# Kernel tuning notes

Measured on AMD Instinct MI355X. Metric: run time of the kernel, lower is better.

## Reference

```python
import jax, jax.numpy as jnp
import numpy as np

N = 100000       # nodes
E = 1600000      # edges
F_IN = 128       # input features
HID = 64         # hidden dim
CLS = 16         # classes


def setup_inputs() -> dict:
    key = jax.random.key(0)
    k = jax.random.split(key, 6)
    x = jax.random.normal(k[0], (N, F_IN), dtype=jnp.float32)
    src = jax.random.randint(k[1], (E,), 0, N, dtype=jnp.int32)
    dst = jax.random.randint(k[2], (E,), 0, N, dtype=jnp.int32)
    edge_index = jnp.stack([src, dst], axis=0)
    W1 = jax.random.normal(k[3], (F_IN, HID), dtype=jnp.float32) * (1.0 / np.sqrt(F_IN))
    b1 = jnp.zeros((HID,), dtype=jnp.float32)
    W2 = jax.random.normal(k[4], (HID, CLS), dtype=jnp.float32) * (1.0 / np.sqrt(HID))
    b2 = jnp.zeros((CLS,), dtype=jnp.float32)
    return {"x": x, "edge_index": edge_index, "W1": W1, "b1": b1, "W2": W2, "b2": b2}


def gcn_conv(x, W, b, src, dst, n_nodes):
    # GCNConv(normalize=True): h = W x; out_i = sum_{j->i} h_j / sqrt(d_i d_j) + h_i / d_i + b
    # (self-loops added with weight 1; deg includes the self-loop)
    h = x @ W                                             # [N, out]
    ones = jnp.ones(src.shape[0], dtype=x.dtype)
    deg = jax.ops.segment_sum(ones, dst, num_segments=n_nodes) + 1.0   # [N]
    dinv = deg ** -0.5
    norm = dinv[src] * dinv[dst]                          # [E]
    msg = h[src] * norm[:, None]                          # [E, out] gather
    out = jax.ops.segment_sum(msg, dst, num_segments=n_nodes)          # scatter-add
    out = out + h * (1.0 / deg)[:, None] + b              # self-loop term + bias
    return out


def reference(x, edge_index, W1, b1, W2, b2):
    src, dst = edge_index[0], edge_index[1]
    n = x.shape[0]
    h = jax.nn.relu(gcn_conv(x, W1, b1, src, dst, n))
    # dropout(p=0.5) is identity in eval mode
    h = jax.nn.relu(gcn_conv(h, W2, b2, src, dst, n))
    return jax.nn.log_softmax(h, axis=-1)
```

## Files before the change

kernel.cpp:

```cpp
#include <hip/hip_runtime.h>
#include <hip/hip_bf16.h>


typedef unsigned short u16;
typedef __attribute__((ext_vector_type(8))) short short8;
typedef __attribute__((ext_vector_type(4))) float f32x4;

#define CAP 4096

__device__ __forceinline__ float bf2f(u16 u) {
  return __uint_as_float(((unsigned int)u) << 16);
}
__device__ __forceinline__ u16 f2bf(float f) {
  unsigned int u = __float_as_uint(f);
  u += 0x7fffu + ((u >> 16) & 1u);
  return (u16)(u >> 16);
}

__global__ __launch_bounds__(256) void kconvw(const void* __restrict__ W1r,
                                              const void* __restrict__ b1r,
                                              const void* __restrict__ W2r,
                                              const void* __restrict__ b2r,
                                              u16* __restrict__ W1b,
                                              float* __restrict__ b1f,
                                              u16* __restrict__ W2b,
                                              float* __restrict__ b2f,
                                              int* __restrict__ mode) {
  __shared__ float red[4];
  __shared__ int smode;
  const u16* w = (const u16*)W1r;
  float mx = 0.f;
  for (int i = threadIdx.x; i < 8192; i += 256) {
    float av = fabsf(bf2f(w[i]));
    if (!(av <= 1e6f)) av = 3e38f;
    mx = fmaxf(mx, av);
  }
  #pragma unroll
  for (int off = 32; off >= 1; off >>= 1) mx = fmaxf(mx, __shfl_xor(mx, off, 64));
  if ((threadIdx.x & 63) == 0) red[threadIdx.x >> 6] = mx;
  __syncthreads();
  if (threadIdx.x == 0) {
    float m2 = fmaxf(fmaxf(red[0], red[1]), fmaxf(red[2], red[3]));
    smode = (m2 > 1e6f) ? 1 : 0;
    if (blockIdx.x == 0) mode[0] = smode;
  }
  __syncthreads();
  int m = smode;
  int gid = blockIdx.x * 256 + threadIdx.x, stride = gridDim.x * 256;
  for (int i = gid; i < 8192; i += stride)
    W1b[i] = m ? f2bf(((const float*)W1r)[i]) : ((const u16*)W1r)[i];
  for (int i = gid; i < 1024; i += stride)
    W2b[i] = m ? f2bf(((const float*)W2r)[i]) : ((const u16*)W2r)[i];
  for (int i = gid; i < 64; i += stride)
    b1f[i] = m ? ((const float*)b1r)[i] : bf2f(((const u16*)b1r)[i]);
  for (int i = gid; i < 16; i += stride)
    b2f[i] = m ? ((const float*)b2r)[i] : bf2f(((const u16*)b2r)[i]);
}

__global__ __launch_bounds__(512) void kpart(const int* __restrict__ src,
                                             const int* __restrict__ dst,
                                             int* __restrict__ cursor,
                                             int* __restrict__ etmp,
                                             int E, int NB) {
  __shared__ int hist[1024], basep[1024];
  int tid = threadIdx.x;
  for (int i = tid; i < 1024; i += 512) hist[i] = 0;
  __syncthreads();
  int e0 = blockIdx.x * 8192 + tid * 16;
  int pk[16], off[16], cb[16];
  if (e0 + 15 < E) {
    int4 s4[4], d4[4];
    #pragma unroll
    for (int u = 0; u < 4; ++u) {
      s4[u] = ((const int4*)(src + e0))[u];
      d4[u] = ((const int4*)(dst + e0))[u];
    }
    const int* sp = (const int*)s4;
    const int* dp = (const int*)d4;
    #pragma unroll
    for (int k = 0; k < 16; ++k) {
      int s = sp[k], d = dp[k];
      cb[k] = d >> 7;
      pk[k] = (s << 7) | (d & 127);
      off[k] = atomicAdd(&hist[cb[k]], 1);
    }
  } else {
    #pragma unroll
    for (int k = 0; k < 16; ++k) {
      int e = e0 + k;
      cb[k] = -1;
      if (e < E) {
        int s = src[e], d = dst[e];
        cb[k] = d >> 7;
        pk[k] = (s << 7) | (d & 127);
        off[k] = atomicAdd(&hist[cb[k]], 1);
      }
    }
  }
  __syncthreads();
  for (int i = tid; i < NB; i += 512)
    if (hist[i]) basep[i] = atomicAdd(&cursor[i], hist[i]);
  __syncthreads();
  if (e0 + 15 < E) {
    #pragma unroll
    for (int k = 0; k < 16; ++k)
      etmp[cb[k] * CAP + basep[cb[k]] + off[k]] = pk[k];
  } else {
    #pragma unroll
    for (int k = 0; k < 16; ++k)
      if (cb[k] >= 0) etmp[cb[k] * CAP + basep[cb[k]] + off[k]] = pk[k];
  }
}

__global__ __launch_bounds__(512) void kfine(const int* __restrict__ etmp,
                                             const int* __restrict__ cursor,
                                             float* __restrict__ dinv, int N) {
  __shared__ int hist[128];
  int bk = blockIdx.x, tid = threadIdx.x;
  int cnt = cursor[bk], base = bk * CAP;
  if (tid < 128) hist[tid] = 0;
  __syncthreads();
  for (int i = tid; i < cnt; i += 512)
    atomicAdd(&hist[etmp[base + i] & 127], 1);
  __syncthreads();
  int node = (bk << 7) + tid;
  if (tid < 128 && node < N)
    dinv[node] = rsqrtf((float)(hist[tid] + 1));
}

__global__ __launch_bounds__(256) void kgemm1(const void* __restrict__ xraw,
                                              const u16* __restrict__ W1b,
                                              const int* __restrict__ mode,
                                              const float* __restrict__ dinv,
                                              u16* __restrict__ h1s, int n) {
  int mflag = mode[0];
  int wid = blockIdx.x * 4 + (threadIdx.x >> 6);
  int row0 = wid * 16;
  if (row0 >= n) return;
  int lane = threadIdx.x & 63;
  int m = lane & 15, q = lane >> 4;

  short8 bfrag[4][4];
  for (int jb = 0; jb < 4; ++jb)
    for (int kb = 0; kb < 4; ++kb) {
      short8 f;
      #pragma unroll
      for (int j = 0; j < 8; ++j)
        f[j] = (short)W1b[(kb * 32 + q * 8 + j) * 64 + jb * 16 + m];
      bfrag[jb][kb] = f;
    }

  f32x4 acc[4];
  #pragma unroll
  for (int jb = 0; jb < 4; ++jb) acc[jb] = (f32x4){0.f, 0.f, 0.f, 0.f};

  #pragma unroll
  for (int kb = 0; kb < 4; ++kb) {
    short8 a;
    if (mflag) {
      const float* xf = (const float*)xraw + (size_t)(row0 + m) * 128 + kb * 32 + q * 8;
      float4 u0 = ((const float4*)xf)[0];
      float4 u1 = ((const float4*)xf)[1];
      __hip_bfloat162 p0 = __float22bfloat162_rn(make_float2(u0.x, u0.y));
      __hip_bfloat162 p1 = __float22bfloat162_rn(make_float2(u0.z, u0.w));
      __hip_bfloat162 p2 = __float22bfloat162_rn(make_float2(u1.x, u1.y));
      __hip_bfloat162 p3 = __float22bfloat162_rn(make_float2(u1.z, u1.w));
      unsigned int w0 = *(const unsigned int*)&p0;
      unsigned int w1 = *(const unsigned int*)&p1;
      unsigned int w2 = *(const unsigned int*)&p2;
      unsigned int w3 = *(const unsigned int*)&p3;
      a[0] = (short)(w0 & 0xffff); a[1] = (short)(w0 >> 16);
      a[2] = (short)(w1 & 0xffff); a[3] = (short)(w1 >> 16);
      a[4] = (short)(w2 & 0xffff); a[5] = (short)(w2 >> 16);
      a[6] = (short)(w3 & 0xffff); a[7] = (short)(w3 >> 16);
    } else {
      a = *(const short8*)((const u16*)xraw + (size_t)(row0 + m) * 128 + kb * 32 + q * 8);
    }
    #pragma unroll
    for (int jb = 0; jb < 4; ++jb)
      acc[jb] = __builtin_amdgcn_mfma_f32_16x16x32_bf16(a, bfrag[jb][kb], acc[jb], 0, 0, 0);
  }

  #pragma unroll
  for (int r = 0; r < 4; ++r) {
    float dv = dinv[row0 + q * 4 + r];
    #pragma unroll
    for (int jb = 0; jb < 4; ++jb)
      h1s[(row0 + q * 4 + r) * 64 + jb * 16 + m] = f2bf(acc[jb][r] * dv);
  }
}

__global__ __launch_bounds__(512) void kagg1f(
    const u16* __restrict__ h1s, const int* __restrict__ etmp,
    const int* __restrict__ cursor, const float* __restrict__ dinv,
    const float* __restrict__ b1f, const u16* __restrict__ W2b,
    int* __restrict__ esort, int2* __restrict__ rowse,
    u16* __restrict__ h2sb, int N) {
  __shared__ int eL[CAP];
  __shared__ int eS[CAP];
  __shared__ int hist[128], starts[128], curs[128];
  __shared__ float sdinv[128];

  int tid = threadIdx.x;
  int bk = blockIdx.x;
  int base = bk * CAP;
  int cnt = cursor[bk];
  int node0 = bk << 7;

  if (tid < 128) {
    hist[tid] = 0;
    int nd = node0 + tid;
    sdinv[tid] = (nd < N) ? dinv[nd] : 0.f;
  }
  __syncthreads();
  for (int i = tid; i < cnt; i += 512) {
    int pk = etmp[base + i];
    eL[i] = pk;
    atomicAdd(&hist[pk & 127], 1);
  }
  __syncthreads();
  if (tid < 64) {
    int v0 = hist[tid], v1 = hist[tid + 64];
    int s0 = v0;
    #pragma unroll
    for (int off = 1; off < 64; off <<= 1) {
      int t = __shfl_up(s0, off, 64);
      if (tid >= off) s0 += t;
    }
    int tot0 = __shfl(s0, 63, 64);
    int s1 = v1;
    #pragma unroll
    for (int off = 1; off < 64; off <<= 1) {
      int t = __shfl_up(s1, off, 64);
      if (tid >= off) s1 += t;
    }
    s1 += tot0;
    int e0x = s0 - v0, e1x = s1 - v1;
    starts[tid] = e0x;  curs[tid] = e0x;
    starts[tid + 64] = e1x;  curs[tid + 64] = e1x;
    int n0 = node0 + tid, n1 = n0 + 64;
    if (n0 < N) rowse[n0] = make_int2(base + e0x, base + e0x + v0);
    if (n1 < N) rowse[n1] = make_int2(base + e1x, base + e1x + v1);
  }
  __syncthreads();
  for (int i = tid; i < cnt; i += 512) {
    int pk = eL[i];
    int pos = atomicAdd(&curs[pk & 127], 1);
    int sidx = pk >> 7;
    eS[pos] = sidx;
    esort[base + pos] = sidx;
  }

  int lane = tid & 63, wv = tid >> 6;
  int m16 = lane & 15, q = lane >> 4;
  short8 bw0, bw1;
  #pragma unroll
  for (int j = 0; j < 8; ++j) {
    bw0[j] = (short)W2b[(q * 8 + j) * 16 + m16];
    bw1[j] = (short)W2b[(32 + q * 8 + j) * 16 + m16];
  }
  __syncthreads();

  float* rowsL = (float*)eL;
  const uint2* h1v = (const uint2*)h1s;
  int ql = m16;

  for (int pass = 0; pass < 4; ++pass) {
    int nl = pass * 32 + wv * 4 + q;
    int nd = node0 + nl;
    int cn = (nd < N) ? nd : node0;
    int rs = starts[nl], deg = hist[nl];
    float a0 = 0.f, a1 = 0.f, a2 = 0.f, a3 = 0.f;
    int k = rs, ke = rs + deg;
    for (; k + 8 <= ke; k += 8) {
      int sI[8];
      uint2 g[8];
      #pragma unroll
      for (int p = 0; p < 8; ++p) sI[p] = eS[k + p];
      #pragma unroll
      for (int p = 0; p < 8; ++p) g[p] = h1v[sI[p] * 16 + ql];
      #pragma unroll
      for (int p = 0; p < 8; ++p) {
        a0 += bf2f((u16)(g[p].x & 0xffff));
        a1 += bf2f((u16)(g[p].x >> 16));
        a2 += bf2f((u16)(g[p].y & 0xffff));
        a3 += bf2f((u16)(g[p].y >> 16));
      }
    }
    for (; k < ke; ++k) {
      int s = eS[k];
      uint2 g = h1v[s * 16 + ql];
      a0 += bf2f((u16)(g.x & 0xffff));
      a1 += bf2f((u16)(g.x >> 16));
      a2 += bf2f((u16)(g.y & 0xffff));
      a3 += bf2f((u16)(g.y >> 16));
    }
    uint2 sg = h1v[cn * 16 + ql];
    float dv = sdinv[nl];
    float4 bv = ((const float4*)b1f)[ql];
    float4 vr;
    vr.x = fmaxf(dv * (a0 + bf2f((u16)(sg.x & 0xffff))) + bv.x, 0.f);
    vr.y = fmaxf(dv * (a1 + bf2f((u16)(sg.x >> 16))) + bv.y, 0.f);
    vr.z = fmaxf(dv * (a2 + bf2f((u16)(sg.y & 0xffff))) + bv.z, 0.f);
    vr.w = fmaxf(dv * (a3 + bf2f((u16)(sg.y >> 16))) + bv.w, 0.f);

    *(float4*)&rowsL[(wv * 4 + q) * 68 + 4 * ql] = vr;
    __builtin_amdgcn_wave_barrier();

    const float* ar = &rowsL[(wv * 4 + (m16 & 3)) * 68];
    bool rv = (m16 < 4);
    short8 af0, af1;
    #pragma unroll
    for (int j = 0; j < 8; ++j) {
      af0[j] = rv ? (short)f2bf(ar[q * 8 + j]) : (short)0;
      af1[j] = rv ? (short)f2bf(ar[32 + q * 8 + j]) : (short)0;
    }
    f32x4 c = (f32x4){0.f, 0.f, 0.f, 0.f};
    c = __builtin_amdgcn_mfma_f32_16x16x32_bf16(af0, bw0, c, 0, 0, 0);
    c = __builtin_amdgcn_mfma_f32_16x16x32_bf16(af1, bw1, c, 0, 0, 0);
    if (q == 0) {
      #pragma unroll
      for (int r = 0; r < 4; ++r) {
        int nl2 = pass * 32 + wv * 4 + r;
        int nd2 = node0 + nl2;
        if (nd2 < N) h2sb[nd2 * 16 + m16] = f2bf(c[r] * sdinv[nl2]);
      }
    }
    __builtin_amdgcn_wave_barrier();
  }
}

__global__ __launch_bounds__(256) void kagg2(
    const u16* __restrict__ h2sb, const int* __restrict__ esort,
    const int2* __restrict__ rowse, const float* __restrict__ dinv,
    const float* __restrict__ b2f, const int* __restrict__ mode,
    void* __restrict__ out, int n) {
  int mflag = mode[0];
  int tid = threadIdx.x;
  int lane = tid & 63, wv = tid >> 6;
  int ol = lane & 7, oc = lane >> 3;
  int node = blockIdx.x * 32 + wv * 8 + oc;
  if (node >= n) node = n - 1;
  int2 se = rowse[node];
  int beg = se.x, end = se.y;
  const unsigned int* h2v = (const unsigned int*)h2sb;
  unsigned int sg = h2v[node * 8 + ol];
  float ax = 0.f, ay = 0.f;

  for (int base = beg; base < end; base += 8) {
    int idx = base + ol;
    int eidx = esort[(idx < end) ? idx : (end - 1)];
    int cnt = min(8, end - base);
    int k = 0;
    for (; k + 8 <= cnt; k += 8) {
      unsigned int g[8];
      #pragma unroll
      for (int p = 0; p < 8; ++p) {
        int s = __shfl(eidx, k + p, 8);
        g[p] = h2v[s * 8 + ol];
      }
      #pragma unroll
      for (int p = 0; p < 8; ++p) {
        ax += bf2f((u16)(g[p] & 0xffff));
        ay += bf2f((u16)(g[p] >> 16));
      }
    }
    for (; k < cnt; ++k) {
      int s = __shfl(eidx, k, 8);
      unsigned int g = h2v[s * 8 + ol];
      ax += bf2f((u16)(g & 0xffff));
      ay += bf2f((u16)(g >> 16));
    }
  }

  float dv = dinv[node];
  float2 b2v = ((const float2*)b2f)[ol];
  float vx = fmaxf(dv * (ax + bf2f((u16)(sg & 0xffff))) + b2v.x, 0.f);
  float vy = fmaxf(dv * (ay + bf2f((u16)(sg >> 16))) + b2v.y, 0.f);

  float m = fmaxf(vx, vy);
  #pragma unroll
  for (int off = 1; off <= 4; off <<= 1) m = fmaxf(m, __shfl_xor(m, off, 8));
  float ex = __expf(vx - m) + __expf(vy - m);
  #pragma unroll
  for (int off = 1; off <= 4; off <<= 1) ex += __shfl_xor(ex, off, 8);
  float lg = __logf(ex);
  float rx = vx - m - lg, ry = vy - m - lg;
  if (mflag) ((float2*)out)[(size_t)node * 8 + ol] = make_float2(rx, ry);
  else ((unsigned int*)out)[(size_t)node * 8 + ol] =
         (unsigned int)f2bf(rx) | ((unsigned int)f2bf(ry) << 16);
}

extern "C" void kernel_launch(void* const* d_in, const int* in_sizes, int n_in,
                              void* d_out, int out_size, void* d_ws, size_t ws_size,
                              hipStream_t stream) {
  const void* x  = d_in[0];
  const int* ei  = (const int*)d_in[1];
  const void* W1 = d_in[2];
  const void* b1 = d_in[3];
  const void* W2 = d_in[4];
  const void* b2 = d_in[5];

  const int N = in_sizes[0] / 128;
  const int E = in_sizes[1] / 2;
  const int* src = ei;
  const int* dst = ei + E;
  const int NB = (N + 127) >> 7;

  char* ws = (char*)d_ws;
  size_t off = 0;
  auto alloc = [&](size_t bytes) -> char* {
    char* p = ws + off;
    off = (off + bytes + 255) & ~(size_t)255;
    return p;
  };
  u16*   h1s    = (u16*)  alloc((size_t)N * 64 * 2);
  u16*   h2sb   = (u16*)  alloc((size_t)N * 16 * 2);
  int*   etmp   = (int*)  alloc((size_t)NB * CAP * 4);
  int*   esort  = (int*)  alloc((size_t)NB * CAP * 4);
  int2*  rowse  = (int2*) alloc((size_t)N * 8);
  float* dinv   = (float*)alloc((size_t)N * 4);
  int*   cursor = (int*)  alloc((size_t)NB * 4);
  u16*   W1b    = (u16*)  alloc(8192 * 2);
  u16*   W2b    = (u16*)  alloc(1024 * 2);
  float* b1f    = (float*)alloc(64 * 4);
  float* b2f    = (float*)alloc(16 * 4);
  int*   mode   = (int*)  alloc(4);

  hipMemsetAsync(cursor, 0, (size_t)NB * 4, stream);

  kconvw<<<32, 256, 0, stream>>>(W1, b1, W2, b2, W1b, b1f, W2b, b2f, mode);

  kpart<<<(E + 8191) / 8192, 512, 0, stream>>>(src, dst, cursor, etmp, E, NB);
  kfine<<<NB, 512, 0, stream>>>(etmp, cursor, dinv, N);

  int tiles = (N + 15) / 16;
  kgemm1<<<(tiles + 3) / 4, 256, 0, stream>>>(x, W1b, mode, dinv, h1s, N);
  kagg1f<<<NB, 512, 0, stream>>>(h1s, etmp, cursor, dinv, b1f, W2b,
                                 esort, rowse, h2sb, N);
  kagg2<<<(N + 31) / 32, 256, 0, stream>>>(h2sb, esort, rowse, dinv, b2f, mode,
                                           d_out, N);
}
```

Measured before the change: 204.9 us.

## Fold weight conversion into partition kernel and widen gather loads in aggregations

The standalone weight/bias conversion kernel is merged into the edge-partition kernel as an extra block 0, removing one kernel launch. In layer-1 aggregation, each node's gather now loads 16-byte rows, two edges at a time per 16-lane group, with a shuffle reduction at the end. Layer-2 aggregation does the same with 8-byte loads and a reworked log-softmax reduction. The aim is fewer, wider memory transactions and more edges in flight, at the cost of extra shuffles and idle lanes on the store path.

```diff
diff --git a/kernel.cpp b/kernel.cpp
--- a/kernel.cpp
+++ b/kernel.cpp
@@ -17,56 +17,51 @@
   return (u16)(u >> 16);
 }
 
-__global__ __launch_bounds__(256) void kconvw(const void* __restrict__ W1r,
-                                              const void* __restrict__ b1r,
-                                              const void* __restrict__ W2r,
-                                              const void* __restrict__ b2r,
-                                              u16* __restrict__ W1b,
-                                              float* __restrict__ b1f,
-                                              u16* __restrict__ W2b,
-                                              float* __restrict__ b2f,
-                                              int* __restrict__ mode) {
-  __shared__ float red[4];
+__global__ __launch_bounds__(512) void kpartc(
+    const int* __restrict__ src, const int* __restrict__ dst,
+    int* __restrict__ cursor, int* __restrict__ etmp,
+    const void* __restrict__ W1r, const void* __restrict__ b1r,
+    const void* __restrict__ W2r, const void* __restrict__ b2r,
+    u16* __restrict__ W1b, float* __restrict__ b1f, u16* __restrict__ W2b,
+    float* __restrict__ b2f, int* __restrict__ mode, int E, int NB) {
+  __shared__ int hist[1024], basep[1024];
+  __shared__ float red[8];
   __shared__ int smode;
-  const u16* w = (const u16*)W1r;
-  float mx = 0.f;
-  for (int i = threadIdx.x; i < 8192; i += 256) {
-    float av = fabsf(bf2f(w[i]));
-    if (!(av <= 1e6f)) av = 3e38f;
-    mx = fmaxf(mx, av);
-  }
-  #pragma unroll
-  for (int off = 32; off >= 1; off >>= 1) mx = fmaxf(mx, __shfl_xor(mx, off, 64));
-  if ((threadIdx.x & 63) == 0) red[threadIdx.x >> 6] = mx;
-  __syncthreads();
-  if (threadIdx.x == 0) {
-    float m2 = fmaxf(fmaxf(red[0], red[1]), fmaxf(red[2], red[3]));
-    smode = (m2 > 1e6f) ? 1 : 0;
-    if (blockIdx.x == 0) mode[0] = smode;
-  }
-  __syncthreads();
-  int m = smode;
-  int gid = blockIdx.x * 256 + threadIdx.x, stride = gridDim.x * 256;
-  for (int i = gid; i < 8192; i += stride)
-    W1b[i] = m ? f2bf(((const float*)W1r)[i]) : ((const u16*)W1r)[i];
-  for (int i = gid; i < 1024; i += stride)
-    W2b[i] = m ? f2bf(((const float*)W2r)[i]) : ((const u16*)W2r)[i];
-  for (int i = gid; i < 64; i += stride)
-    b1f[i] = m ? ((const float*)b1r)[i] : bf2f(((const u16*)b1r)[i]);
-  for (int i = gid; i < 16; i += stride)
-    b2f[i] = m ? ((const float*)b2r)[i] : bf2f(((const u16*)b2r)[i]);
-}
-
-__global__ __launch_bounds__(512) void kpart(const int* __restrict__ src,
-                                             const int* __restrict__ dst,
-                                             int* __restrict__ cursor,
-                                             int* __restrict__ etmp,
-                                             int E, int NB) {
-  __shared__ int hist[1024], basep[1024];
   int tid = threadIdx.x;
+
+  if (blockIdx.x == 0) {
+    const u16* w = (const u16*)W1r;
+    float mx = 0.f;
+    for (int i = tid; i < 8192; i += 512) {
+      float av = fabsf(bf2f(w[i]));
+      if (!(av <= 1e6f)) av = 3e38f;
+      mx = fmaxf(mx, av);
+    }
+    #pragma unroll
+    for (int off = 32; off >= 1; off >>= 1) mx = fmaxf(mx, __shfl_xor(mx, off, 64));
+    if ((tid & 63) == 0) red[tid >> 6] = mx;
+    __syncthreads();
+    if (tid == 0) {
+      float m2 = 0.f;
+      #pragma unroll
+      for (int wv = 0; wv < 8; ++wv) m2 = fmaxf(m2, red[wv]);
+      smode = (m2 > 1e6f) ? 1 : 0;
+      mode[0] = smode;
+    }
+    __syncthreads();
+    int m = smode;
+    for (int i = tid; i < 8192; i += 512)
+      W1b[i] = m ? f2bf(((const float*)W1r)[i]) : ((const u16*)W1r)[i];
+    for (int i = tid; i < 1024; i += 512)
+      W2b[i] = m ? f2bf(((const float*)W2r)[i]) : ((const u16*)W2r)[i];
+    if (tid < 64) b1f[tid] = m ? ((const float*)b1r)[tid] : bf2f(((const u16*)b1r)[tid]);
+    if (tid < 16) b2f[tid] = m ? ((const float*)b2r)[tid] : bf2f(((const u16*)b2r)[tid]);
+    return;
+  }
+
   for (int i = tid; i < 1024; i += 512) hist[i] = 0;
   __syncthreads();
-  int e0 = blockIdx.x * 8192 + tid * 16;
+  int e0 = (blockIdx.x - 1) * 8192 + tid * 16;
   int pk[16], off[16], cb[16];
   if (e0 + 15 < E) {
     int4 s4[4], d4[4];
@@ -262,49 +257,76 @@
   __syncthreads();
 
   float* rowsL = (float*)eL;
-  const uint2* h1v = (const uint2*)h1s;
-  int ql = m16;
+  const uint4* h1u = (const uint4*)h1s;
+  int fl = m16 & 7, hl = m16 >> 3;
+  int wrow = wv * 4 + q;
 
   for (int pass = 0; pass < 4; ++pass) {
     int nl = pass * 32 + wv * 4 + q;
     int nd = node0 + nl;
     int cn = (nd < N) ? nd : node0;
-    int rs = starts[nl], deg = hist[nl];
+    int rs = starts[nl], ke = rs + hist[nl];
     float a0 = 0.f, a1 = 0.f, a2 = 0.f, a3 = 0.f;
-    int k = rs, ke = rs + deg;
+    float a4 = 0.f, a5 = 0.f, a6 = 0.f, a7 = 0.f;
+    int k = rs;
     for (; k + 8 <= ke; k += 8) {
-      int sI[8];
-      uint2 g[8];
-      #pragma unroll
-      for (int p = 0; p < 8; ++p) sI[p] = eS[k + p];
-      #pragma unroll
-      for (int p = 0; p < 8; ++p) g[p] = h1v[sI[p] * 16 + ql];
-      #pragma unroll
-      for (int p = 0; p < 8; ++p) {
-        a0 += bf2f((u16)(g[p].x & 0xffff));
-        a1 += bf2f((u16)(g[p].x >> 16));
-        a2 += bf2f((u16)(g[p].y & 0xffff));
-        a3 += bf2f((u16)(g[p].y >> 16));
+      int i0 = eS[k + hl], i1 = eS[k + 2 + hl];
+      int i2 = eS[k + 4 + hl], i3 = eS[k + 6 + hl];
+      uint4 g0 = h1u[i0 * 8 + fl];
+      uint4 g1 = h1u[i1 * 8 + fl];
+      uint4 g2 = h1u[i2 * 8 + fl];
+      uint4 g3 = h1u[i3 * 8 + fl];
+      a0 += bf2f((u16)(g0.x & 0xffff)) + bf2f((u16)(g1.x & 0xffff))
+          + bf2f((u16)(g2.x & 0xffff)) + bf2f((u16)(g3.x & 0xffff));
+      a1 += bf2f((u16)(g0.x >> 16)) + bf2f((u16)(g1.x >> 16))
+          + bf2f((u16)(g2.x >> 16)) + bf2f((u16)(g3.x >> 16));
+      a2 += bf2f((u16)(g0.y & 0xffff)) + bf2f((u16)(g1.y & 0xffff))
+          + bf2f((u16)(g2.y & 0xffff)) + bf2f((u16)(g3.y & 0xffff));
+      a3 += bf2f((u16)(g0.y >> 16)) + bf2f((u16)(g1.y >> 16))
+          + bf2f((u16)(g2.y >> 16)) + bf2f((u16)(g3.y >> 16));
+      a4 += bf2f((u16)(g0.z & 0xffff)) + bf2f((u16)(g1.z & 0xffff))
+          + bf2f((u16)(g2.z & 0xffff)) + bf2f((u16)(g3.z & 0xffff));
+      a5 += bf2f((u16)(g0.z >> 16)) + bf2f((u16)(g1.z >> 16))
+          + bf2f((u16)(g2.z >> 16)) + bf2f((u16)(g3.z >> 16));
+      a6 += bf2f((u16)(g0.w & 0xffff)) + bf2f((u16)(g1.w & 0xffff))
+          + bf2f((u16)(g2.w & 0xffff)) + bf2f((u16)(g3.w & 0xffff));
+      a7 += bf2f((u16)(g0.w >> 16)) + bf2f((u16)(g1.w >> 16))
+          + bf2f((u16)(g2.w >> 16)) + bf2f((u16)(g3.w >> 16));
+    }
+    for (; k < ke; k += 2) {
+      int e = k + hl;
+      bool valid = e < ke;
+      uint4 g = h1u[eS[valid ? e : (ke - 1)] * 8 + fl];
+      if (valid) {
+        a0 += bf2f((u16)(g.x & 0xffff));  a1 += bf2f((u16)(g.x >> 16));
+        a2 += bf2f((u16)(g.y & 0xffff));  a3 += bf2f((u16)(g.y >> 16));
+        a4 += bf2f((u16)(g.z & 0xffff));  a5 += bf2f((u16)(g.z >> 16));
+        a6 += bf2f((u16)(g.w & 0xffff));  a7 += bf2f((u16)(g.w >> 16));
       }
     }
-    for (; k < ke; ++k) {
-      int s = eS[k];
-      uint2 g = h1v[s * 16 + ql];
-      a0 += bf2f((u16)(g.x & 0xffff));
-      a1 += bf2f((u16)(g.x >> 16));
-      a2 += bf2f((u16)(g.y & 0xffff));
-      a3 += bf2f((u16)(g.y >> 16));
-    }
-    uint2 sg = h1v[cn * 16 + ql];
+    a0 += __shfl_xor(a0, 8, 16);  a1 += __shfl_xor(a1, 8, 16);
+    a2 += __shfl_xor(a2, 8, 16);  a3 += __shfl_xor(a3, 8, 16);
+    a4 += __shfl_xor(a4, 8, 16);  a5 += __shfl_xor(a5, 8, 16);
+    a6 += __shfl_xor(a6, 8, 16);  a7 += __shfl_xor(a7, 8, 16);
+
+    uint4 sg = h1u[cn * 8 + fl];
     float dv = sdinv[nl];
-    float4 bv = ((const float4*)b1f)[ql];
-    float4 vr;
-    vr.x = fmaxf(dv * (a0 + bf2f((u16)(sg.x & 0xffff))) + bv.x, 0.f);
-    vr.y = fmaxf(dv * (a1 + bf2f((u16)(sg.x >> 16))) + bv.y, 0.f);
-    vr.z = fmaxf(dv * (a2 + bf2f((u16)(sg.y & 0xffff))) + bv.z, 0.f);
-    vr.w = fmaxf(dv * (a3 + bf2f((u16)(sg.y >> 16))) + bv.w, 0.f);
-
-    *(float4*)&rowsL[(wv * 4 + q) * 68 + 4 * ql] = vr;
+    float4 ba = ((const float4*)b1f)[2 * fl];
+    float4 bb = ((const float4*)b1f)[2 * fl + 1];
+    float v0 = fmaxf(dv * (a0 + bf2f((u16)(sg.x & 0xffff))) + ba.x, 0.f);
+    float v1 = fmaxf(dv * (a1 + bf2f((u16)(sg.x >> 16))) + ba.y, 0.f);
+    float v2 = fmaxf(dv * (a2 + bf2f((u16)(sg.y & 0xffff))) + ba.z, 0.f);
+    float v3 = fmaxf(dv * (a3 + bf2f((u16)(sg.y >> 16))) + ba.w, 0.f);
+    float v4 = fmaxf(dv * (a4 + bf2f((u16)(sg.z & 0xffff))) + bb.x, 0.f);
+    float v5 = fmaxf(dv * (a5 + bf2f((u16)(sg.z >> 16))) + bb.y, 0.f);
+    float v6 = fmaxf(dv * (a6 + bf2f((u16)(sg.w & 0xffff))) + bb.z, 0.f);
+    float v7 = fmaxf(dv * (a7 + bf2f((u16)(sg.w >> 16))) + bb.w, 0.f);
+
+    if (hl == 0) {
+      float* rp = &rowsL[wrow * 68 + 8 * fl];
+      *(float4*)rp = make_float4(v0, v1, v2, v3);
+      *(float4*)(rp + 4) = make_float4(v4, v5, v6, v7);
+    }
     __builtin_amdgcn_wave_barrier();
 
     const float* ar = &rowsL[(wv * 4 + (m16 & 3)) * 68];
@@ -338,57 +360,71 @@
   int mflag = mode[0];
   int tid = threadIdx.x;
   int lane = tid & 63, wv = tid >> 6;
-  int ol = lane & 7, oc = lane >> 3;
+  int oc = lane >> 3, ol = lane & 7;
+  int hl = ol >> 2, fl = ol & 3;
   int node = blockIdx.x * 32 + wv * 8 + oc;
   if (node >= n) node = n - 1;
   int2 se = rowse[node];
   int beg = se.x, end = se.y;
-  const unsigned int* h2v = (const unsigned int*)h2sb;
-  unsigned int sg = h2v[node * 8 + ol];
-  float ax = 0.f, ay = 0.f;
-
-  for (int base = beg; base < end; base += 8) {
-    int idx = base + ol;
-    int eidx = esort[(idx < end) ? idx : (end - 1)];
-    int cnt = min(8, end - base);
-    int k = 0;
-    for (; k + 8 <= cnt; k += 8) {
-      unsigned int g[8];
-      #pragma unroll
-      for (int p = 0; p < 8; ++p) {
-        int s = __shfl(eidx, k + p, 8);
-        g[p] = h2v[s * 8 + ol];
-      }
-      #pragma unroll
-      for (int p = 0; p < 8; ++p) {
-        ax += bf2f((u16)(g[p] & 0xffff));
-        ay += bf2f((u16)(g[p] >> 16));
-      }
-    }
-    for (; k < cnt; ++k) {
-      int s = __shfl(eidx, k, 8);
-      unsigned int g = h2v[s * 8 + ol];
-      ax += bf2f((u16)(g & 0xffff));
-      ay += bf2f((u16)(g >> 16));
-    }
-  }
+  const uint2* h2v = (const uint2*)h2sb;
+  uint2 sg = h2v[node * 4 + fl];
+  float a0 = 0.f, a1 = 0.f, a2 = 0.f, a3 = 0.f;
+
+  int k = beg;
+  for (; k + 8 <= end; k += 8) {
+    int i0 = esort[k + hl], i1 = esort[k + 2 + hl];
+    int i2 = esort[k + 4 + hl], i3 = esort[k + 6 + hl];
+    uint2 g0 = h2v[i0 * 4 + fl];
+    uint2 g1 = h2v[i1 * 4 + fl];
+    uint2 g2 = h2v[i2 * 4 + fl];
+    uint2 g3 = h2v[i3 * 4 + fl];
+    a0 += bf2f((u16)(g0.x & 0xffff)) + bf2f((u16)(g1.x & 0xffff))
+        + bf2f((u16)(g2.x & 0xffff)) + bf2f((u16)(g3.x & 0xffff));
+    a1 += bf2f((u16)(g0.x >> 16)) + bf2f((u16)(g1.x >> 16))
+        + bf2f((u16)(g2.x >> 16)) + bf2f((u16)(g3.x >> 16));
+    a2 += bf2f((u16)(g0.y & 0xffff)) + bf2f((u16)(g1.y & 0xffff))
+        + bf2f((u16)(g2.y & 0xffff)) + bf2f((u16)(g3.y & 0xffff));
+    a3 += bf2f((u16)(g0.y >> 16)) + bf2f((u16)(g1.y >> 16))
+        + bf2f((u16)(g2.y >> 16)) + bf2f((u16)(g3.y >> 16));
+  }
+  for (; k < end; k += 2) {
+    int e = k + hl;
+    bool valid = e < end;
+    uint2 g = h2v[esort[valid ? e : (end - 1)] * 4 + fl];
+    if (valid) {
+      a0 += bf2f((u16)(g.x & 0xffff));  a1 += bf2f((u16)(g.x >> 16));
+      a2 += bf2f((u16)(g.y & 0xffff));  a3 += bf2f((u16)(g.y >> 16));
+    }
+  }
+  a0 += __shfl_xor(a0, 4, 8);  a1 += __shfl_xor(a1, 4, 8);
+  a2 += __shfl_xor(a2, 4, 8);  a3 += __shfl_xor(a3, 4, 8);
 
   float dv = dinv[node];
-  float2 b2v = ((const float2*)b2f)[ol];
-  float vx = fmaxf(dv * (ax + bf2f((u16)(sg & 0xffff))) + b2v.x, 0.f);
-  float vy = fmaxf(dv * (ay + bf2f((u16)(sg >> 16))) + b2v.y, 0.f);
-
-  float m = fmaxf(vx, vy);
-  #pragma unroll
-  for (int off = 1; off <= 4; off <<= 1) m = fmaxf(m, __shfl_xor(m, off, 8));
-  float ex = __expf(vx - m) + __expf(vy - m);
-  #pragma unroll
-  for (int off = 1; off <= 4; off <<= 1) ex += __shfl_xor(ex, off, 8);
+  float4 bv = ((const float4*)b2f)[fl];
+  float v0 = fmaxf(dv * (a0 + bf2f((u16)(sg.x & 0xffff))) + bv.x, 0.f);
+  float v1 = fmaxf(dv * (a1 + bf2f((u16)(sg.x >> 16))) + bv.y, 0.f);
+  float v2 = fmaxf(dv * (a2 + bf2f((u16)(sg.y & 0xffff))) + bv.z, 0.f);
+  float v3 = fmaxf(dv * (a3 + bf2f((u16)(sg.y >> 16))) + bv.w, 0.f);
+
+  float m = fmaxf(fmaxf(v0, v1), fmaxf(v2, v3));
+  m = fmaxf(m, __shfl_xor(m, 1, 4));
+  m = fmaxf(m, __shfl_xor(m, 2, 4));
+  float ex = __expf(v0 - m) + __expf(v1 - m) + __expf(v2 - m) + __expf(v3 - m);
+  ex += __shfl_xor(ex, 1, 4);
+  ex += __shfl_xor(ex, 2, 4);
   float lg = __logf(ex);
-  float rx = vx - m - lg, ry = vy - m - lg;
-  if (mflag) ((float2*)out)[(size_t)node * 8 + ol] = make_float2(rx, ry);
-  else ((unsigned int*)out)[(size_t)node * 8 + ol] =
-         (unsigned int)f2bf(rx) | ((unsigned int)f2bf(ry) << 16);
+  float r0 = v0 - m - lg, r1 = v1 - m - lg;
+  float r2 = v2 - m - lg, r3 = v3 - m - lg;
+  if (hl == 0) {
+    if (mflag) {
+      ((float4*)out)[(size_t)node * 4 + fl] = make_float4(r0, r1, r2, r3);
+    } else {
+      uint2 o;
+      o.x = (unsigned int)f2bf(r0) | ((unsigned int)f2bf(r1) << 16);
+      o.y = (unsigned int)f2bf(r2) | ((unsigned int)f2bf(r3) << 16);
+      ((uint2*)out)[(size_t)node * 4 + fl] = o;
+    }
+  }
 }
 
 extern "C" void kernel_launch(void* const* d_in, const int* in_sizes, int n_in,
@@ -429,9 +465,10 @@
 
   hipMemsetAsync(cursor, 0, (size_t)NB * 4, stream);
 
-  kconvw<<<32, 256, 0, stream>>>(W1, b1, W2, b2, W1b, b1f, W2b, b2f, mode);
-
-  kpart<<<(E + 8191) / 8192, 512, 0, stream>>>(src, dst, cursor, etmp, E, NB);
+  int pblocks = (E + 8191) / 8192;
+  kpartc<<<pblocks + 1, 512, 0, stream>>>(src, dst, cursor, etmp,
+                                          W1, b1, W2, b2,
+                                          W1b, b1f, W2b, b2f, mode, E, NB);
   kfine<<<NB, 512, 0, stream>>>(etmp, cursor, dinv, N);
 
   int tiles = (N + 15) / 16;
```

New measurement: 197.6 us. -3.6%, faster.
